# Kernel tuning notes

Measured on AMD Instinct MI355X. Metric: run time of the kernel, lower is better.

Reference implementation:

```python
import jax, jax.numpy as jnp
import numpy as np

N_NODES = 512   # nodes per graph == feature dim (GCNConv in_channels)
B = 64          # batch of graphs
HID = 16        # action_hidden_dim == edge_hidden_dim
E = 262144      # total edges (~8 per node)
N_TOTAL = B * N_NODES


def _gcn(x, W, b, src, dst, n):
    """PyG GCNConv: add self loops, sym-normalize, x@W -> scatter-add, +bias."""
    h = x @ W  # [n, hid]
    loop = jnp.arange(n)
    s = jnp.concatenate([src, loop])
    d = jnp.concatenate([dst, loop])
    deg = jax.ops.segment_sum(jnp.ones((s.shape[0],), x.dtype), d, num_segments=n)
    dinv = jnp.where(deg > 0, jax.lax.rsqrt(deg), 0.0)
    norm = dinv[s] * dinv[d]
    out = jax.ops.segment_sum(norm[:, None] * h[s], d, num_segments=n)
    return out + b


def _group_sum(t, ptr):
    # cumsum-based segment sum over contiguous node blocks, as in the original
    c = jnp.concatenate([jnp.zeros((1,) + t.shape[1:], t.dtype), jnp.cumsum(t, axis=0)], axis=0)
    return c[ptr[1:]] - c[ptr[:-1]]


def setup_inputs() -> dict:
    key = jax.random.key(0)
    k = jax.random.split(key, 4)
    node_feature = jax.random.normal(k[0], (N_TOTAL, N_NODES), jnp.float32)
    edge_index = jax.random.randint(k[1], (E, 2), 0, N_TOTAL)  # global node ids
    node_index = jnp.arange(N_TOTAL)                            # sorted global ids
    batch_ptr = jnp.arange(B + 1) * N_NODES
    scale = np.float32(1.0 / np.sqrt(N_NODES))
    W_act = jax.random.normal(k[2], (N_NODES, HID), jnp.float32) * scale
    b_act = jnp.zeros((HID,), jnp.float32)
    W_edge = jax.random.normal(k[3], (N_NODES, HID), jnp.float32) * scale
    b_edge = jnp.zeros((HID,), jnp.float32)
    return {"node_feature": node_feature, "W_act": W_act, "b_act": b_act,
            "W_edge": W_edge, "b_edge": b_edge, "edge_index": edge_index,
            "node_index": node_index, "batch_ptr": batch_ptr}


def reference(node_feature, W_act, b_act, W_edge, b_edge, edge_index, node_index, batch_ptr):
    n_total, n_nodes = node_feature.shape
    n_graphs = batch_ptr.shape[0] - 1
    # remap global ids -> local positions; node_index sorted => searchsorted
    # is exactly the original's torch.where(edge_index[...,None]==node_index)[2]
    ei = jnp.searchsorted(node_index, edge_index)  # [E, 2]
    src, dst = ei[:, 0], ei[:, 1]
    # action-type head: GCN -> mean over hidden -> per-graph segment sum
    at = _gcn(node_feature, W_act, b_act, src, dst, n_total)          # [N, hid]
    at = _group_sum(jnp.mean(at, axis=-1, keepdims=True), batch_ptr)  # [B, 1]
    # edge head: GCN -> per-graph pairwise inner products
    eh = _gcn(node_feature, W_edge, b_edge, src, dst, n_total)
    eh = eh.reshape(n_graphs, n_nodes, -1)                            # [B, n, hid]
    pair = jnp.einsum('bnf,bmf->bnm', eh, eh)                         # [B, n, n]
    edge_actions = pair.reshape(n_graphs, n_nodes * n_nodes)
    return jnp.concatenate([at, edge_actions], axis=-1)               # [B, 1 + n*n]
```

## Files before the change

### kernel.cpp

```cpp
#include <hip/hip_runtime.h>
#include <stdint.h>

#define NTOT   32768
#define NNODE  512
#define NGRAPH 64
#define HID    16
#define NEDGE  262144
#define OROW   262145
#define CAP    32

typedef __attribute__((ext_vector_type(4)))  float f32x4;
typedef __attribute__((ext_vector_type(16))) float f32x16;
typedef __attribute__((ext_vector_type(8)))  short bf16x8;

static __device__ __forceinline__ unsigned short f2bf(float f) {
  union { float f; unsigned int u; } v; v.f = f;
  unsigned int u = v.u;
  u += 0x7fffu + ((u >> 16) & 1u);
  return (unsigned short)(u >> 16);
}

__global__ void k_init(const float* __restrict__ Wa,
                       const float* __restrict__ We,
                       unsigned short* __restrict__ Wtc,
                       int* __restrict__ cnt, float* __restrict__ out) {
  int t = blockIdx.x * 256 + threadIdx.x;
  cnt[t] = 0;
  if (t < NGRAPH) out[(size_t)t * OROW] = 0.0f;
  if (t < 16384) {
    int c = t & 31, k = t >> 5;
    float v = (c < 16) ? Wa[k * 16 + c] : We[k * 16 + (c - 16)];
    Wtc[c * 512 + k] = f2bf(v);
  }
}

__global__ void k_fill(const int* __restrict__ ei, int* __restrict__ cnt,
                       int* __restrict__ csr) {
  int e = blockIdx.x * 256 + threadIdx.x;
  int2 sd = ((const int2*)ei)[e];
  int pos = atomicAdd(&cnt[sd.y], 1);
  if (pos < CAP) csr[sd.y * CAP + pos] = sd.x;
}

__global__ __launch_bounds__(256) void k_gemm(const float* __restrict__ x,
                                              const unsigned short* __restrict__ Wtc,
                                              float* __restrict__ h_act,
                                              float* __restrict__ h_edge) {
  int wave = threadIdx.x >> 6, lane = threadIdx.x & 63;
  int tile = blockIdx.x * 4 + wave;
  int row0 = tile * 32;
  int r = lane & 31, g = lane >> 5;
  const float* xp = x + (size_t)(row0 + r) * 512 + g * 8;
  const unsigned short* bp = Wtc + r * 512 + g * 8;
  f32x16 acc = {0,0,0,0,0,0,0,0,0,0,0,0,0,0,0,0};
  #pragma unroll 8
  for (int kb = 0; kb < 32; ++kb) {
    f32x4 x0 = *(const f32x4*)(xp + kb * 16);
    f32x4 x1 = *(const f32x4*)(xp + kb * 16 + 4);
    bf16x8 a;
    #pragma unroll
    for (int j = 0; j < 4; ++j) {
      a[j]     = (short)f2bf(x0[j]);
      a[j + 4] = (short)f2bf(x1[j]);
    }
    bf16x8 bb = *(const bf16x8*)(bp + kb * 16);
    acc = __builtin_amdgcn_mfma_f32_32x32x16_bf16(a, bb, acc, 0, 0, 0);
  }
  float* hp = (r < 16) ? h_act : h_edge;
  int c = r & 15;
  #pragma unroll
  for (int i = 0; i < 16; ++i) {
    int row = row0 + (i & 3) + 8 * (i >> 2) + 4 * g;
    hp[row * HID + c] = acc[i];
  }
}

__global__ __launch_bounds__(256) void k_gather(const int* __restrict__ cnt,
                                                const int* __restrict__ csr,
                                                const float* __restrict__ h_act,
                                                const float* __restrict__ h_edge,
                                                const float* __restrict__ ba,
                                                const float* __restrict__ be,
                                                unsigned short* __restrict__ ebf,
                                                float* __restrict__ out) {
  int tid = blockIdx.x * 256 + threadIdx.x;
  int node = tid >> 4, f = tid & 15;
  int deg = cnt[node];
  float dd = rsqrtf(1.0f + (float)deg);
  int nd = min(deg, CAP);
  float w0 = dd * dd;
  float acc_a = w0 * h_act[(size_t)node * HID + f];
  float acc_e = w0 * h_edge[(size_t)node * HID + f];
  const int* bucket = csr + (size_t)node * CAP;
  for (int k = 0; k < nd; ++k) {
    int s = bucket[k];
    float w = rsqrtf(1.0f + (float)cnt[s]) * dd;
    acc_a += w * h_act[(size_t)s * HID + f];
    acc_e += w * h_edge[(size_t)s * HID + f];
  }
  float va = acc_a + ba[f];
  float ve = acc_e + be[f];
  ebf[tid] = f2bf(ve);
  #pragma unroll
  for (int m = 1; m < 16; m <<= 1) va += __shfl_xor(va, m, 64);
  if (f == 0)
    unsafeAtomicAdd(out + (size_t)(node >> 9) * OROW, va * (1.0f / 16.0f));
}

__global__ __launch_bounds__(256) void k_gram(const unsigned short* __restrict__ ebf,
                                              float* __restrict__ out) {
  int b = blockIdx.x;
  int graph = b >> 3, sub = b & 7;
  int wave = threadIdx.x >> 6, lane = threadIdx.x & 63;
  int r = lane & 15, g = lane >> 4;
  int n0 = (sub * 4 + wave) * 16;
  const unsigned short* eb = ebf + graph * NNODE * HID;
  size_t obase = (size_t)graph * OROW + 1;
  bf16x8 zf = {0,0,0,0,0,0,0,0};
  bf16x8 a = zf;
  if (g < 2) a = *(const bf16x8*)(eb + (n0 + r) * HID + g * 8);
  for (int mt = 0; mt < 32; ++mt) {
    int m0 = mt * 16;
    bf16x8 bb = zf;
    if (g < 2) bb = *(const bf16x8*)(eb + (m0 + r) * HID + g * 8);
    f32x4 acc = {0, 0, 0, 0};
    acc = __builtin_amdgcn_mfma_f32_16x16x32_bf16(a, bb, acc, 0, 0, 0);
    #pragma unroll
    for (int j = 0; j < 4; ++j) {
      int n = n0 + g * 4 + j;
      out[obase + (size_t)n * NNODE + m0 + r] = acc[j];
    }
  }
}

extern "C" void kernel_launch(void* const* d_in, const int* in_sizes, int n_in,
                              void* d_out, int out_size, void* d_ws, size_t ws_size,
                              hipStream_t stream) {
  const float* x  = (const float*)d_in[0];
  const float* Wa = (const float*)d_in[1];
  const float* ba = (const float*)d_in[2];
  const float* We = (const float*)d_in[3];
  const float* be = (const float*)d_in[4];
  const int* ei   = (const int*)d_in[5];
  float* out = (float*)d_out;

  char* w = (char*)d_ws;
  float* h_act    = (float*)(w);
  float* h_edge   = (float*)(w + (2u << 20));
  unsigned short* ebf = (unsigned short*)(w + (4u << 20));
  int*   csr      = (int*)  (w + (5u << 20));
  int*   cnt      = (int*)  (w + (9u << 20));
  unsigned short* Wtc = (unsigned short*)(w + (9u << 20) + (128u << 10));

  k_init  <<<128, 256, 0, stream>>>(Wa, We, Wtc, cnt, out);
  k_fill  <<<1024, 256, 0, stream>>>(ei, cnt, csr);
  k_gemm  <<<256, 256, 0, stream>>>(x, Wtc, h_act, h_edge);
  k_gather<<<2048, 256, 0, stream>>>(cnt, csr, h_act, h_edge, ba, be, ebf, out);
  k_gram  <<<512, 256, 0, stream>>>(ebf, out);
}
```

Baseline: 72.89 us.

## Fuse CSR fill into split-K GEMM kernel and drop init kernel

Replaces the init, fill and GEMM kernels with a memset plus one combined kernel. Its first 1024 blocks each compute 32 rows with split-K over 8 waves, reduced through shared memory, and its remaining blocks build the CSR buckets with two edges per thread. The weight transpose/bf16 conversion kernel is dropped: weights are read and packed inline. The per-graph action sum now goes block-reduced into a workspace array and is written into the output by the gram kernel. This cuts launch count and gives the GEMM more parallelism, at the cost of 33KB of LDS per block and redundant strided weight loads.

```diff
diff --git a/kernel.cpp b/kernel.cpp
--- a/kernel.cpp
+++ b/kernel.cpp
@@ -1,4 +1,5 @@
 #include <hip/hip_runtime.h>
+#include <hip/hip_bf16.h>
 #include <stdint.h>
 
 #define NTOT   32768
@@ -8,11 +9,19 @@
 #define NEDGE  262144
 #define OROW   262145
 #define CAP    32
+#define GEMM_BLOCKS 1024
 
 typedef __attribute__((ext_vector_type(4)))  float f32x4;
 typedef __attribute__((ext_vector_type(16))) float f32x16;
 typedef __attribute__((ext_vector_type(8)))  short bf16x8;
 
+union U8 { bf16x8 v; unsigned int u[4]; };
+
+static __device__ __forceinline__ unsigned int pkbf(float lo, float hi) {
+  union { __hip_bfloat162 h; unsigned int u; } c;
+  c.h = __float22bfloat162_rn(float2{lo, hi});
+  return c.u;
+}
 static __device__ __forceinline__ unsigned short f2bf(float f) {
   union { float f; unsigned int u; } v; v.f = f;
   unsigned int u = v.u;
@@ -20,59 +29,62 @@
   return (unsigned short)(u >> 16);
 }
 
-__global__ void k_init(const float* __restrict__ Wa,
-                       const float* __restrict__ We,
-                       unsigned short* __restrict__ Wtc,
-                       int* __restrict__ cnt, float* __restrict__ out) {
-  int t = blockIdx.x * 256 + threadIdx.x;
-  cnt[t] = 0;
-  if (t < NGRAPH) out[(size_t)t * OROW] = 0.0f;
-  if (t < 16384) {
-    int c = t & 31, k = t >> 5;
-    float v = (c < 16) ? Wa[k * 16 + c] : We[k * 16 + (c - 16)];
-    Wtc[c * 512 + k] = f2bf(v);
+__global__ __launch_bounds__(512) void k_gemmfill(const float* __restrict__ x,
+                                                  const float* __restrict__ Wa,
+                                                  const float* __restrict__ We,
+                                                  const int* __restrict__ ei,
+                                                  int* __restrict__ cnt,
+                                                  int* __restrict__ csr,
+                                                  float* __restrict__ h_act,
+                                                  float* __restrict__ h_edge) {
+  __shared__ float red[64 * 129];
+  if (blockIdx.x >= GEMM_BLOCKS) {
+    int i = (blockIdx.x - GEMM_BLOCKS) * 512 + threadIdx.x;
+    int4 e2 = ((const int4*)ei)[i];
+    int p0 = atomicAdd(&cnt[e2.y], 1);
+    if (p0 < CAP) csr[e2.y * CAP + p0] = e2.x;
+    int p1 = atomicAdd(&cnt[e2.w], 1);
+    if (p1 < CAP) csr[e2.w * CAP + p1] = e2.z;
+    return;
   }
-}
-
-__global__ void k_fill(const int* __restrict__ ei, int* __restrict__ cnt,
-                       int* __restrict__ csr) {
-  int e = blockIdx.x * 256 + threadIdx.x;
-  int2 sd = ((const int2*)ei)[e];
-  int pos = atomicAdd(&cnt[sd.y], 1);
-  if (pos < CAP) csr[sd.y * CAP + pos] = sd.x;
-}
-
-__global__ __launch_bounds__(256) void k_gemm(const float* __restrict__ x,
-                                              const unsigned short* __restrict__ Wtc,
-                                              float* __restrict__ h_act,
-                                              float* __restrict__ h_edge) {
-  int wave = threadIdx.x >> 6, lane = threadIdx.x & 63;
-  int tile = blockIdx.x * 4 + wave;
-  int row0 = tile * 32;
+  int row0 = blockIdx.x * 32;
+  int w = threadIdx.x >> 6, lane = threadIdx.x & 63;
   int r = lane & 31, g = lane >> 5;
-  const float* xp = x + (size_t)(row0 + r) * 512 + g * 8;
-  const unsigned short* bp = Wtc + r * 512 + g * 8;
+  const float* xp = x + (size_t)(row0 + r) * 512 + w * 64 + g * 8;
+  const float* Wp = ((r < 16) ? Wa : We) + (r & 15);
+  int k0 = w * 64 + g * 8;
   f32x16 acc = {0,0,0,0,0,0,0,0,0,0,0,0,0,0,0,0};
-  #pragma unroll 8
-  for (int kb = 0; kb < 32; ++kb) {
+  #pragma unroll
+  for (int kb = 0; kb < 4; ++kb) {
     f32x4 x0 = *(const f32x4*)(xp + kb * 16);
     f32x4 x1 = *(const f32x4*)(xp + kb * 16 + 4);
-    bf16x8 a;
+    U8 a, b;
+    a.u[0] = pkbf(x0[0], x0[1]);
+    a.u[1] = pkbf(x0[2], x0[3]);
+    a.u[2] = pkbf(x1[0], x1[1]);
+    a.u[3] = pkbf(x1[2], x1[3]);
+    int kk = k0 + kb * 16;
     #pragma unroll
-    for (int j = 0; j < 4; ++j) {
-      a[j]     = (short)f2bf(x0[j]);
-      a[j + 4] = (short)f2bf(x1[j]);
-    }
-    bf16x8 bb = *(const bf16x8*)(bp + kb * 16);
-    acc = __builtin_amdgcn_mfma_f32_32x32x16_bf16(a, bb, acc, 0, 0, 0);
+    for (int p = 0; p < 4; ++p)
+      b.u[p] = pkbf(Wp[(kk + 2 * p) * 16], Wp[(kk + 2 * p + 1) * 16]);
+    acc = __builtin_amdgcn_mfma_f32_32x32x16_bf16(a.v, b.v, acc, 0, 0, 0);
   }
-  float* hp = (r < 16) ? h_act : h_edge;
-  int c = r & 15;
   #pragma unroll
-  for (int i = 0; i < 16; ++i) {
-    int row = row0 + (i & 3) + 8 * (i >> 2) + 4 * g;
-    hp[row * HID + c] = acc[i];
+  for (int i = 0; i < 16; ++i) red[lane * 129 + w * 16 + i] = acc[i];
+  __syncthreads();
+  int rl = threadIdx.x & 63, q = threadIdx.x >> 6;
+  float s0 = 0.f, s1 = 0.f;
+  #pragma unroll
+  for (int ww = 0; ww < 8; ++ww) {
+    s0 += red[rl * 129 + ww * 16 + q * 2];
+    s1 += red[rl * 129 + ww * 16 + q * 2 + 1];
   }
+  int col = rl & 31, gg = rl >> 5;
+  float* hp = (col < 16) ? h_act : h_edge;
+  int c = col & 15;
+  int i0 = q * 2, i1 = i0 + 1;
+  hp[(row0 + (i0 & 3) + 8 * (i0 >> 2) + 4 * gg) * HID + c] = s0;
+  hp[(row0 + (i1 & 3) + 8 * (i1 >> 2) + 4 * gg) * HID + c] = s1;
 }
 
 __global__ __launch_bounds__(256) void k_gather(const int* __restrict__ cnt,
@@ -82,7 +94,7 @@
                                                 const float* __restrict__ ba,
                                                 const float* __restrict__ be,
                                                 unsigned short* __restrict__ ebf,
-                                                float* __restrict__ out) {
+                                                float* __restrict__ at_graph) {
   int tid = blockIdx.x * 256 + threadIdx.x;
   int node = tid >> 4, f = tid & 15;
   int deg = cnt[node];
@@ -103,14 +115,24 @@
   ebf[tid] = f2bf(ve);
   #pragma unroll
   for (int m = 1; m < 16; m <<= 1) va += __shfl_xor(va, m, 64);
-  if (f == 0)
-    unsafeAtomicAdd(out + (size_t)(node >> 9) * OROW, va * (1.0f / 16.0f));
+  __shared__ float ablk[16];
+  if (f == 0) ablk[threadIdx.x >> 4] = va;
+  __syncthreads();
+  if (threadIdx.x == 0) {
+    float s = 0.f;
+    #pragma unroll
+    for (int i = 0; i < 16; ++i) s += ablk[i];
+    unsafeAtomicAdd(&at_graph[blockIdx.x >> 5], s);
+  }
 }
 
 __global__ __launch_bounds__(256) void k_gram(const unsigned short* __restrict__ ebf,
+                                              const float* __restrict__ at_graph,
                                               float* __restrict__ out) {
   int b = blockIdx.x;
   int graph = b >> 3, sub = b & 7;
+  if (sub == 0 && threadIdx.x == 0)
+    out[(size_t)graph * OROW] = at_graph[graph] * (1.0f / 16.0f);
   int wave = threadIdx.x >> 6, lane = threadIdx.x & 63;
   int r = lane & 15, g = lane >> 4;
   int n0 = (sub * 4 + wave) * 16;
@@ -150,11 +172,10 @@
   unsigned short* ebf = (unsigned short*)(w + (4u << 20));
   int*   csr      = (int*)  (w + (5u << 20));
   int*   cnt      = (int*)  (w + (9u << 20));
-  unsigned short* Wtc = (unsigned short*)(w + (9u << 20) + (128u << 10));
+  float* at_graph = (float*)(w + (9u << 20) + (128u << 10));
 
-  k_init  <<<128, 256, 0, stream>>>(Wa, We, Wtc, cnt, out);
-  k_fill  <<<1024, 256, 0, stream>>>(ei, cnt, csr);
-  k_gemm  <<<256, 256, 0, stream>>>(x, Wtc, h_act, h_edge);
-  k_gather<<<2048, 256, 0, stream>>>(cnt, csr, h_act, h_edge, ba, be, ebf, out);
-  k_gram  <<<512, 256, 0, stream>>>(ebf, out);
+  hipMemsetAsync(cnt, 0, 32768 * 4 + 64 * 4, stream);
+  k_gemmfill<<<1280, 512, 0, stream>>>(x, Wa, We, ei, cnt, csr, h_act, h_edge);
+  k_gather  <<<2048, 256, 0, stream>>>(cnt, csr, h_act, h_edge, ba, be, ebf, at_graph);
+  k_gram    <<<512, 256, 0, stream>>>(ebf, at_graph, out);
 }
```

Measured after the change: 72.13 us. Within noise of the previous version (-1.0%).
